# Kernel optimization log

Hardware: AMD Instinct MI355X
Metric: run time of the kernel (lower is better)

The kernel has to match this reference:

```python
import jax, jax.numpy as jnp
import numpy as np

B, S, H = 2, 2048, 1024
NUM_HEAD = 16
HEAD = H // NUM_HEAD
NEG = -10000000000.0


def setup_inputs() -> dict:
    key = jax.random.key(0)
    ks = jax.random.split(key, 10)
    scale = 1.0 / np.sqrt(H)
    return {
        "query": jax.random.normal(ks[0], (B, S, H), jnp.float32),
        "key": jax.random.normal(ks[1], (B, S, H), jnp.float32),
        "value": jax.random.normal(ks[2], (B, S, H), jnp.float32),
        "mask": jax.random.randint(ks[3], (B, S), 0, 2, jnp.int32),
        "Wq": jax.random.normal(ks[4], (H, H), jnp.float32) * scale,
        "bq": jnp.zeros((H,), jnp.float32),
        "Wk": jax.random.normal(ks[5], (H, H), jnp.float32) * scale,
        "bk": jnp.zeros((H,), jnp.float32),
        "Wv": jax.random.normal(ks[6], (H, H), jnp.float32) * scale,
        "bv": jnp.zeros((H,), jnp.float32),
    }


def reference(query, key, value, mask, Wq, bq, Wk, bk, Wv, bv):
    b, s, h = query.shape
    # Linear projections (torch Linear: x @ W.T + b), split into heads -> [b, nh, s, hd]
    def proj(x, W, bias):
        y = x @ W.T + bias
        return y.reshape(b, s, NUM_HEAD, HEAD).transpose(0, 2, 1, 3)

    q = proj(query, Wq, bq)
    k = proj(key, Wk, bk)
    v = proj(value, Wv, bv)

    # NOTE: original module has NO 1/sqrt(head_dim) scaling -- faithful.
    attn_score = jnp.einsum("bhqd,bhkd->bhqk", q, k)  # [b, nh, s, s]
    # key-padding mask bias: 0 where mask==1, -1e10 where mask==0, broadcast over query dim
    bias_add = jnp.where(mask[:, None, None, :] == 0, NEG, 0.0).astype(attn_score.dtype)
    attn_score = attn_score + bias_add
    attn_ratio = jax.nn.softmax(attn_score, axis=-1)
    out = jnp.einsum("bhqk,bhkd->bhqd", attn_ratio, v)  # [b, nh, s, hd]
    out = out.transpose(0, 2, 1, 3).reshape(b, s, h)
    # Dropout is identity in eval mode; output_linear is defined but never used in forward.
    return out
```

## Files before the change

### kernel.cpp

```cpp
#include <hip/hip_runtime.h>

#define BATCH 2
#define S_LEN 2048
#define HDIM  1024
#define NHEAD 16
#define HD    64
#define NEGBIAS -1e10f
#define LOG2E 1.44269504088896f

typedef __attribute__((ext_vector_type(8))) _Float16 half8;
typedef __attribute__((ext_vector_type(4))) _Float16 half4;
typedef __attribute__((ext_vector_type(4))) float   f32x4;
typedef __attribute__((ext_vector_type(2))) __fp16 fp16x2;
typedef __attribute__((ext_vector_type(4))) __fp16 fp16x4;
typedef __attribute__((ext_vector_type(8))) __fp16 fp16x8;

__device__ __forceinline__ float max3f(float a, float b, float c) {
    return fmaxf(fmaxf(a, b), c);
}

__global__ __launch_bounds__(256) void proj_gemm_f16(
    const float* __restrict__ Xq, const float* __restrict__ Wq, const float* __restrict__ bq,
    const float* __restrict__ Xk, const float* __restrict__ Wk, const float* __restrict__ bk,
    const float* __restrict__ Xv, const float* __restrict__ Wv, const float* __restrict__ bv,
    _Float16* __restrict__ Qb, _Float16* __restrict__ Kb, _Float16* __restrict__ Vtb)
{
    const int l  = blockIdx.x;
    const int x  = l & 7;
    const int j  = l >> 3;
    const int mt_ = x * 4 + (j & 3);
    const int nt_ = (j >> 2) & 7;
    const int z   = j >> 5;

    const float* X    = (z == 0) ? Xq : (z == 1) ? Xk : Xv;
    const float* W    = (z == 0) ? Wq : (z == 1) ? Wk : Wv;
    const float* bias = (z == 0) ? bq : (z == 1) ? bk : bv;
    _Float16* Y       = (z == 0) ? Qb : (z == 1) ? Kb : Vtb;

    const int n0 = nt_ * 128;
    const int m0 = mt_ * 128;

    __shared__ __align__(16) _Float16 As[128][40];
    __shared__ __align__(16) _Float16 Bs[128][40];

    const int t    = threadIdx.x;
    const int w    = t >> 6;
    const int lane = t & 63;
    const int quad = lane >> 4;
    const int lc   = lane & 15;
    const int wm   = (w >> 1) * 64;
    const int wn   = (w & 1) * 64;

    const f32x4 fzero = {0.f, 0.f, 0.f, 0.f};
    f32x4 acc[4][4];
#pragma unroll
    for (int i = 0; i < 4; i++)
#pragma unroll
        for (int j2 = 0; j2 < 4; j2++) acc[i][j2] = fzero;

    const int srow = t >> 2;
    const int sc   = t & 3;

    float4 xa0[2][2], wa0[2][2], xa1[2][2], wa1[2][2];

#define PROJ_ISSUE(K0, XA, WA)                                                \
    {                                                                         \
        _Pragma("unroll")                                                     \
        for (int hf = 0; hf < 2; hf++) {                                      \
            const float* gx = X + (size_t)(m0 + srow + hf * 64) * HDIM + (K0) + sc * 8; \
            XA[hf][0] = *(const float4*)gx;                                   \
            XA[hf][1] = *(const float4*)(gx + 4);                             \
            const float* gw = W + (size_t)(n0 + srow + hf * 64) * HDIM + (K0) + sc * 8; \
            WA[hf][0] = *(const float4*)gw;                                   \
            WA[hf][1] = *(const float4*)(gw + 4);                             \
        }                                                                     \
    }

#define PK8(dst, f0, f1)                                                      \
    {                                                                         \
        fp16x2 p0 = __builtin_amdgcn_cvt_pkrtz((f0).x, (f0).y);               \
        fp16x2 p1 = __builtin_amdgcn_cvt_pkrtz((f0).z, (f0).w);               \
        fp16x2 p2 = __builtin_amdgcn_cvt_pkrtz((f1).x, (f1).y);               \
        fp16x2 p3 = __builtin_amdgcn_cvt_pkrtz((f1).z, (f1).w);               \
        fp16x4 lo = __builtin_shufflevector(p0, p1, 0, 1, 2, 3);              \
        fp16x4 hi = __builtin_shufflevector(p2, p3, 0, 1, 2, 3);              \
        fp16x8 v8 = __builtin_shufflevector(lo, hi, 0, 1, 2, 3, 4, 5, 6, 7);  \
        dst = __builtin_bit_cast(half8, v8);                                  \
    }

#define PROJ_STAGE(XA, WA)                                                    \
    {                                                                         \
        _Pragma("unroll")                                                     \
        for (int hf = 0; hf < 2; hf++) {                                      \
            int row = srow + hf * 64;                                         \
            half8 vx, vw;                                                     \
            PK8(vx, XA[hf][0], XA[hf][1])                                     \
            PK8(vw, WA[hf][0], WA[hf][1])                                     \
            *(half8*)&As[row][sc * 8] = vx;                                   \
            *(half8*)&Bs[row][sc * 8] = vw;                                   \
        }                                                                     \
    }

#define PROJ_COMPUTE                                                          \
    {                                                                         \
        half8 af[4], bf[4];                                                   \
        _Pragma("unroll")                                                     \
        for (int mt = 0; mt < 4; mt++)                                        \
            af[mt] = *(const half8*)&As[wm + mt * 16 + lc][quad * 8];         \
        _Pragma("unroll")                                                     \
        for (int nt = 0; nt < 4; nt++)                                        \
            bf[nt] = *(const half8*)&Bs[wn + nt * 16 + lc][quad * 8];         \
        _Pragma("unroll")                                                     \
        for (int mt = 0; mt < 4; mt++)                                        \
            _Pragma("unroll")                                                 \
            for (int nt = 0; nt < 4; nt++)                                    \
                acc[mt][nt] = __builtin_amdgcn_mfma_f32_16x16x32_f16(         \
                    af[mt], bf[nt], acc[mt][nt], 0, 0, 0);                    \
    }

    PROJ_ISSUE(0,  xa0, wa0)
    PROJ_ISSUE(32, xa1, wa1)

    for (int k0 = 0; k0 < HDIM; k0 += 64) {
        if (k0) __syncthreads();
        PROJ_STAGE(xa0, wa0)
        __syncthreads();
        if (k0 + 64 < HDIM) PROJ_ISSUE(k0 + 64, xa0, wa0)
        PROJ_COMPUTE

        __syncthreads();
        PROJ_STAGE(xa1, wa1)
        __syncthreads();
        if (k0 + 96 < HDIM) PROJ_ISSUE(k0 + 96, xa1, wa1)
        PROJ_COMPUTE
    }

#pragma unroll
    for (int nt = 0; nt < 4; nt++) {
        const int n = n0 + wn + nt * 16 + lc;
        const float bv_ = bias[n];
        const int h = n >> 6, d = n & 63;
#pragma unroll
        for (int mt = 0; mt < 4; mt++) {
#pragma unroll
            for (int r = 0; r < 4; r++) {
                const int m = m0 + wm + mt * 16 + quad * 4 + r;
                const int b = m >> 11, s = m & (S_LEN - 1);
                const int bh = b * NHEAD + h;
                float y = acc[mt][nt][r] + bv_;
                if (z == 0) y *= LOG2E;
                _Float16 val = (_Float16)y;
                if (z == 2)
                    Y[((size_t)bh * HD + d) * S_LEN + s] = val;
                else
                    Y[((size_t)bh * S_LEN + s) * HD + d] = val;
            }
        }
    }
}

__global__ __launch_bounds__(256) void flash_attn_mfma(
    const _Float16* __restrict__ Qb, const _Float16* __restrict__ Kb,
    const _Float16* __restrict__ Vtb, const int* __restrict__ mask,
    float* __restrict__ out)
{
    const int bid = blockIdx.x;
    const int swz = (bid & 7) * 64 + (bid >> 3);
    const int qt = swz & 15;
    const int bh = swz >> 4;
    const int b  = bh >> 4;
    const int h  = bh & (NHEAD - 1);

    __shared__ __align__(16) _Float16 Ks [64][72];
    __shared__ __align__(16) _Float16 Vts[64][72];
    __shared__ __align__(16) _Float16 Ps [4][32][72];
    __shared__ float biasS[64];

    const int t    = threadIdx.x;
    const int w    = t >> 6;
    const int lane = t & 63;
    const int quad = lane >> 4;
    const int lc   = lane & 15;

    const _Float16* Kbase = Kb  + (size_t)bh * S_LEN * HD;
    const _Float16* Vbase = Vtb + (size_t)bh * HD * S_LEN;
    const int* mbase = mask + b * S_LEN;

    half8 qf[2][2];
#pragma unroll
    for (int qg = 0; qg < 2; qg++) {
        const int qrow = qt * 128 + w * 32 + qg * 16 + lc;
#pragma unroll
        for (int s = 0; s < 2; s++)
            qf[qg][s] = *(const half8*)(Qb + ((size_t)bh * S_LEN + qrow) * HD
                                        + s * 32 + quad * 8);
    }

    f32x4 o[2][4];
    const f32x4 fzero = {0.f, 0.f, 0.f, 0.f};
#pragma unroll
    for (int qg = 0; qg < 2; qg++)
#pragma unroll
        for (int nt = 0; nt < 4; nt++) o[qg][nt] = fzero;
    float mrun[2] = {-3.0e38f, -3.0e38f};
    float lrun[2] = {0.f, 0.f};

    const int rr0 = t >> 3,          cc0 = (t & 7) * 8;
    const int rr1 = (t + 256) >> 3;

    half8 kpre[2], vpre[2];
    int   mpre;
#define ATTN_ISSUE(KT)                                                        \
    {                                                                         \
        kpre[0] = *(const half8*)(Kbase + (size_t)((KT) + rr0) * HD + cc0);   \
        kpre[1] = *(const half8*)(Kbase + (size_t)((KT) + rr1) * HD + cc0);   \
        vpre[0] = *(const half8*)(Vbase + (size_t)rr0 * S_LEN + (KT) + cc0);  \
        vpre[1] = *(const half8*)(Vbase + (size_t)rr1 * S_LEN + (KT) + cc0);  \
        mpre    = mbase[(KT) + (t & 63)];                                     \
    }

    ATTN_ISSUE(0)

    for (int kt = 0; kt < S_LEN; kt += 64) {
        if (kt) __syncthreads();
        *(half8*)&Ks [rr0][cc0] = kpre[0];
        *(half8*)&Ks [rr1][cc0] = kpre[1];
        *(half8*)&Vts[rr0][cc0] = vpre[0];
        *(half8*)&Vts[rr1][cc0] = vpre[1];
        if (t < 64) biasS[t] = mpre ? 0.f : NEGBIAS;
        __syncthreads();

        if (kt + 64 < S_LEN) ATTN_ISSUE(kt + 64)

        f32x4 scf[2][4];
#pragma unroll
        for (int tt = 0; tt < 4; tt++) {
            float4 b4 = *(const float4*)&biasS[tt * 16 + quad * 4];
            f32x4 cini = {b4.x, b4.y, b4.z, b4.w};
            scf[0][tt] = cini;
            scf[1][tt] = cini;
        }
#pragma unroll
        for (int s = 0; s < 2; s++) {
#pragma unroll
            for (int tt = 0; tt < 4; tt++) {
                half8 kf = *(const half8*)&Ks[tt * 16 + lc][s * 32 + quad * 8];
                scf[0][tt] = __builtin_amdgcn_mfma_f32_16x16x32_f16(kf, qf[0][s], scf[0][tt], 0, 0, 0);
                scf[1][tt] = __builtin_amdgcn_mfma_f32_16x16x32_f16(kf, qf[1][s], scf[1][tt], 0, 0, 0);
            }
        }

#pragma unroll
        for (int qg = 0; qg < 2; qg++) {
            const f32x4 a0 = scf[qg][0], a1 = scf[qg][1],
                        a2 = scf[qg][2], a3 = scf[qg][3];
            float m0 = max3f(a0[0], a0[1], a0[2]);
            float m1 = max3f(a0[3], a1[0], a1[1]);
            float m2 = max3f(a1[2], a1[3], a2[0]);
            float m3 = max3f(a2[1], a2[2], a2[3]);
            float m4 = max3f(a3[0], a3[1], a3[2]);
            float mx = fmaxf(max3f(m0, m1, m2), max3f(m3, m4, a3[3]));
            mx = fmaxf(mx, __shfl_xor(mx, 16));
            mx = fmaxf(mx, __shfl_xor(mx, 32));

            if (!__all(mx <= mrun[qg] + 8.f)) {
                float mn = fmaxf(mrun[qg], mx);
                float al = __builtin_amdgcn_exp2f(mrun[qg] - mn);
                lrun[qg] *= al;
#pragma unroll
                for (int nt = 0; nt < 4; nt++) {
                    o[qg][nt][0] *= al; o[qg][nt][1] *= al;
                    o[qg][nt][2] *= al; o[qg][nt][3] *= al;
                }
                mrun[qg] = mn;
            }

            const float mr = mrun[qg];
            float ps[4][4];
#pragma unroll
            for (int tt = 0; tt < 4; tt++)
#pragma unroll
                for (int r = 0; r < 4; r++) {
                    float p = __builtin_amdgcn_exp2f(scf[qg][tt][r] - mr);
                    ps[tt][r] = p;
                }
            float s0 = (ps[0][0] + ps[0][1]) + (ps[0][2] + ps[0][3]);
            float s1 = (ps[1][0] + ps[1][1]) + (ps[1][2] + ps[1][3]);
            float s2 = (ps[2][0] + ps[2][1]) + (ps[2][2] + ps[2][3]);
            float s3 = (ps[3][0] + ps[3][1]) + (ps[3][2] + ps[3][3]);
            float ls = (s0 + s1) + (s2 + s3);
            ls += __shfl_xor(ls, 16);
            ls += __shfl_xor(ls, 32);
            lrun[qg] += ls;

#pragma unroll
            for (int tt = 0; tt < 4; tt++) {
                fp16x2 p01 = __builtin_amdgcn_cvt_pkrtz(ps[tt][0], ps[tt][1]);
                fp16x2 p23 = __builtin_amdgcn_cvt_pkrtz(ps[tt][2], ps[tt][3]);
                fp16x4 pk4 = __builtin_shufflevector(p01, p23, 0, 1, 2, 3);
                *(half4*)&Ps[w][qg * 16 + lc][tt * 16 + quad * 4] =
                    __builtin_bit_cast(half4, pk4);
            }
        }

#pragma unroll
        for (int s = 0; s < 2; s++) {
            half8 pf0 = *(const half8*)&Ps[w][lc]     [s * 32 + quad * 8];
            half8 pf1 = *(const half8*)&Ps[w][16 + lc][s * 32 + quad * 8];
#pragma unroll
            for (int nt = 0; nt < 4; nt++) {
                half8 vf = *(const half8*)&Vts[nt * 16 + lc][s * 32 + quad * 8];
                o[0][nt] = __builtin_amdgcn_mfma_f32_16x16x32_f16(vf, pf0, o[0][nt], 0, 0, 0);
                o[1][nt] = __builtin_amdgcn_mfma_f32_16x16x32_f16(vf, pf1, o[1][nt], 0, 0, 0);
            }
        }
    }

#pragma unroll
    for (int qg = 0; qg < 2; qg++) {
        const int qrow = qt * 128 + w * 32 + qg * 16 + lc;
        const float inv = 1.f / lrun[qg];
        const size_t rowb = ((size_t)b * S_LEN + qrow) * HDIM + h * HD;
#pragma unroll
        for (int nt = 0; nt < 4; nt++) {
            float4 v;
            v.x = o[qg][nt][0] * inv; v.y = o[qg][nt][1] * inv;
            v.z = o[qg][nt][2] * inv; v.w = o[qg][nt][3] * inv;
            *(float4*)&out[rowb + nt * 16 + quad * 4] = v;
        }
    }
}

extern "C" void kernel_launch(void* const* d_in, const int* in_sizes, int n_in,
                              void* d_out, int out_size, void* d_ws, size_t ws_size,
                              hipStream_t stream) {
    const float* query = (const float*)d_in[0];
    const float* key   = (const float*)d_in[1];
    const float* value = (const float*)d_in[2];
    const int*   mask  = (const int*)  d_in[3];
    const float* Wq    = (const float*)d_in[4];
    const float* bq    = (const float*)d_in[5];
    const float* Wk    = (const float*)d_in[6];
    const float* bk    = (const float*)d_in[7];
    const float* Wv    = (const float*)d_in[8];
    const float* bv    = (const float*)d_in[9];
    float* out = (float*)d_out;

    const size_t nElem = (size_t)BATCH * S_LEN * HDIM;
    if (ws_size < 3 * nElem * sizeof(_Float16)) return;
    _Float16* Qb  = (_Float16*)d_ws;
    _Float16* Kb  = Qb + nElem;
    _Float16* Vtb = Kb + nElem;

    proj_gemm_f16<<<768, 256, 0, stream>>>(query, Wq, bq, key, Wk, bk,
                                           value, Wv, bv, Qb, Kb, Vtb);

    flash_attn_mfma<<<BATCH * NHEAD * (S_LEN / 128), 256, 0, stream>>>(
        Qb, Kb, Vtb, mask, out);
}
```

Measured before the change: 236.3 us.

## Stage projection GEMM tiles via direct global-to-LDS loads with XOR swizzle

The QKV projection GEMM now copies fp32 X and W tiles straight from global memory into LDS with global_load_lds, double-buffered, instead of loading into registers, converting to fp16 and then storing to LDS. The fp16 conversion moves to the LDS read side, and a XOR swizzle on columns is meant to avoid bank conflicts. The goal is to cut register pressure and the number of barriers per k-step, and to let loads overlap with MFMA work. In exchange, LDS use doubles because it holds fp32 and two buffers, and every wave repeats the conversion work on each read.

```diff
diff --git a/kernel.cpp b/kernel.cpp
--- a/kernel.cpp
+++ b/kernel.cpp
@@ -18,6 +18,24 @@
 __device__ __forceinline__ float max3f(float a, float b, float c) {
     return fmaxf(fmaxf(a, b), c);
 }
+
+__device__ __forceinline__ void gload16(const float* g, float* l) {
+    __builtin_amdgcn_global_load_lds(
+        (const __attribute__((address_space(1))) unsigned int*)g,
+        (__attribute__((address_space(3))) unsigned int*)l, 16, 0, 0);
+}
+
+#define PK8V(dst, lo, hi)                                                     \
+    {                                                                         \
+        fp16x2 p0 = __builtin_amdgcn_cvt_pkrtz((lo)[0], (lo)[1]);             \
+        fp16x2 p1 = __builtin_amdgcn_cvt_pkrtz((lo)[2], (lo)[3]);             \
+        fp16x2 p2 = __builtin_amdgcn_cvt_pkrtz((hi)[0], (hi)[1]);             \
+        fp16x2 p3 = __builtin_amdgcn_cvt_pkrtz((hi)[2], (hi)[3]);             \
+        fp16x4 l4 = __builtin_shufflevector(p0, p1, 0, 1, 2, 3);              \
+        fp16x4 h4 = __builtin_shufflevector(p2, p3, 0, 1, 2, 3);              \
+        fp16x8 v8 = __builtin_shufflevector(l4, h4, 0, 1, 2, 3, 4, 5, 6, 7);  \
+        dst = __builtin_bit_cast(half8, v8);                                  \
+    }
 
 __global__ __launch_bounds__(256) void proj_gemm_f16(
     const float* __restrict__ Xq, const float* __restrict__ Wq, const float* __restrict__ bq,
@@ -40,8 +58,8 @@
     const int n0 = nt_ * 128;
     const int m0 = mt_ * 128;
 
-    __shared__ __align__(16) _Float16 As[128][40];
-    __shared__ __align__(16) _Float16 Bs[128][40];
+    __shared__ __align__(16) float As[2][128 * 32];
+    __shared__ __align__(16) float Bs[2][128 * 32];
 
     const int t    = threadIdx.x;
     const int w    = t >> 6;
@@ -58,58 +76,42 @@
 #pragma unroll
         for (int j2 = 0; j2 < 4; j2++) acc[i][j2] = fzero;
 
-    const int srow = t >> 2;
-    const int sc   = t & 3;
-
-    float4 xa0[2][2], wa0[2][2], xa1[2][2], wa1[2][2];
-
-#define PROJ_ISSUE(K0, XA, WA)                                                \
+    const int lr  = lane >> 3;
+    const int lcx = (lane & 7) ^ lr;
+    const float* gA = X + (size_t)(m0 + w * 32 + lr) * HDIM + lcx * 4;
+    const float* gB = W + (size_t)(n0 + w * 32 + lr) * HDIM + lcx * 4;
+    const int ach = w * 1024;
+
+#define PROJ_STAGE(BUF, K0)                                                   \
     {                                                                         \
         _Pragma("unroll")                                                     \
-        for (int hf = 0; hf < 2; hf++) {                                      \
-            const float* gx = X + (size_t)(m0 + srow + hf * 64) * HDIM + (K0) + sc * 8; \
-            XA[hf][0] = *(const float4*)gx;                                   \
-            XA[hf][1] = *(const float4*)(gx + 4);                             \
-            const float* gw = W + (size_t)(n0 + srow + hf * 64) * HDIM + (K0) + sc * 8; \
-            WA[hf][0] = *(const float4*)gw;                                   \
-            WA[hf][1] = *(const float4*)(gw + 4);                             \
+        for (int c = 0; c < 4; c++) {                                         \
+            gload16(gA + (K0) + c * 8192, &As[BUF][ach + c * 256]);           \
+            gload16(gB + (K0) + c * 8192, &Bs[BUF][ach + c * 256]);           \
         }                                                                     \
     }
 
-#define PK8(dst, f0, f1)                                                      \
-    {                                                                         \
-        fp16x2 p0 = __builtin_amdgcn_cvt_pkrtz((f0).x, (f0).y);               \
-        fp16x2 p1 = __builtin_amdgcn_cvt_pkrtz((f0).z, (f0).w);               \
-        fp16x2 p2 = __builtin_amdgcn_cvt_pkrtz((f1).x, (f1).y);               \
-        fp16x2 p3 = __builtin_amdgcn_cvt_pkrtz((f1).z, (f1).w);               \
-        fp16x4 lo = __builtin_shufflevector(p0, p1, 0, 1, 2, 3);              \
-        fp16x4 hi = __builtin_shufflevector(p2, p3, 0, 1, 2, 3);              \
-        fp16x8 v8 = __builtin_shufflevector(lo, hi, 0, 1, 2, 3, 4, 5, 6, 7);  \
-        dst = __builtin_bit_cast(half8, v8);                                  \
-    }
-
-#define PROJ_STAGE(XA, WA)                                                    \
-    {                                                                         \
-        _Pragma("unroll")                                                     \
-        for (int hf = 0; hf < 2; hf++) {                                      \
-            int row = srow + hf * 64;                                         \
-            half8 vx, vw;                                                     \
-            PK8(vx, XA[hf][0], XA[hf][1])                                     \
-            PK8(vw, WA[hf][0], WA[hf][1])                                     \
-            *(half8*)&As[row][sc * 8] = vx;                                   \
-            *(half8*)&Bs[row][sc * 8] = vw;                                   \
-        }                                                                     \
-    }
-
-#define PROJ_COMPUTE                                                          \
+    const int xr   = lc & 7;
+    const int arow = (wm + lc) * 32;
+    const int brow = (wn + lc) * 32;
+    const int ac0  = ((quad * 2)     ^ xr) * 4;
+    const int ac1  = ((quad * 2 + 1) ^ xr) * 4;
+
+#define PROJ_COMPUTE(BUF)                                                     \
     {                                                                         \
         half8 af[4], bf[4];                                                   \
         _Pragma("unroll")                                                     \
-        for (int mt = 0; mt < 4; mt++)                                        \
-            af[mt] = *(const half8*)&As[wm + mt * 16 + lc][quad * 8];         \
+        for (int mt = 0; mt < 4; mt++) {                                      \
+            f32x4 lo = *(const f32x4*)&As[BUF][arow + mt * 512 + ac0];        \
+            f32x4 hi = *(const f32x4*)&As[BUF][arow + mt * 512 + ac1];        \
+            PK8V(af[mt], lo, hi)                                              \
+        }                                                                     \
         _Pragma("unroll")                                                     \
-        for (int nt = 0; nt < 4; nt++)                                        \
-            bf[nt] = *(const half8*)&Bs[wn + nt * 16 + lc][quad * 8];         \
+        for (int nt = 0; nt < 4; nt++) {                                      \
+            f32x4 lo = *(const f32x4*)&Bs[BUF][brow + nt * 512 + ac0];        \
+            f32x4 hi = *(const f32x4*)&Bs[BUF][brow + nt * 512 + ac1];        \
+            PK8V(bf[nt], lo, hi)                                              \
+        }                                                                     \
         _Pragma("unroll")                                                     \
         for (int mt = 0; mt < 4; mt++)                                        \
             _Pragma("unroll")                                                 \
@@ -118,21 +120,16 @@
                     af[mt], bf[nt], acc[mt][nt], 0, 0, 0);                    \
     }
 
-    PROJ_ISSUE(0,  xa0, wa0)
-    PROJ_ISSUE(32, xa1, wa1)
+    PROJ_STAGE(0, 0)
+    __syncthreads();
 
     for (int k0 = 0; k0 < HDIM; k0 += 64) {
-        if (k0) __syncthreads();
-        PROJ_STAGE(xa0, wa0)
+        if (k0 + 32 < HDIM) PROJ_STAGE(1, k0 + 32)
+        PROJ_COMPUTE(0)
         __syncthreads();
-        if (k0 + 64 < HDIM) PROJ_ISSUE(k0 + 64, xa0, wa0)
-        PROJ_COMPUTE
-
+        if (k0 + 64 < HDIM) PROJ_STAGE(0, k0 + 64)
+        PROJ_COMPUTE(1)
         __syncthreads();
-        PROJ_STAGE(xa1, wa1)
-        __syncthreads();
-        if (k0 + 96 < HDIM) PROJ_ISSUE(k0 + 96, xa1, wa1)
-        PROJ_COMPUTE
     }
 
 #pragma unroll
```

After: 253.7 us. 7.4% more time.

## Double-buffer LDS in projection GEMM and use a plain 3D launch grid

Applied to the files above, without the earlier changes.

The projection GEMM now keeps two LDS buffers for the A and B tiles. This cuts the barriers per 64-wide k step from four to two, and the next global loads are issued before each barrier rather than after it. The swizzled 1D block index mapping is replaced by a plain 3D grid (n tile, m tile, which projection), which changes the order in which blocks touch X and W in L2. LDS use per block doubles, which may lower occupancy, and the new block order could hurt cache locality compared with the old swizzle.

```diff
diff --git a/kernel.cpp b/kernel.cpp
--- a/kernel.cpp
+++ b/kernel.cpp
@@ -19,29 +19,34 @@
     return fmaxf(fmaxf(a, b), c);
 }
 
+__device__ __forceinline__ half8 pk8(float4 a, float4 b) {
+    fp16x2 p0 = __builtin_amdgcn_cvt_pkrtz(a.x, a.y);
+    fp16x2 p1 = __builtin_amdgcn_cvt_pkrtz(a.z, a.w);
+    fp16x2 p2 = __builtin_amdgcn_cvt_pkrtz(b.x, b.y);
+    fp16x2 p3 = __builtin_amdgcn_cvt_pkrtz(b.z, b.w);
+    fp16x4 lo = __builtin_shufflevector(p0, p1, 0, 1, 2, 3);
+    fp16x4 hi = __builtin_shufflevector(p2, p3, 0, 1, 2, 3);
+    fp16x8 v8 = __builtin_shufflevector(lo, hi, 0, 1, 2, 3, 4, 5, 6, 7);
+    return __builtin_bit_cast(half8, v8);
+}
+
 __global__ __launch_bounds__(256) void proj_gemm_f16(
     const float* __restrict__ Xq, const float* __restrict__ Wq, const float* __restrict__ bq,
     const float* __restrict__ Xk, const float* __restrict__ Wk, const float* __restrict__ bk,
     const float* __restrict__ Xv, const float* __restrict__ Wv, const float* __restrict__ bv,
     _Float16* __restrict__ Qb, _Float16* __restrict__ Kb, _Float16* __restrict__ Vtb)
 {
-    const int l  = blockIdx.x;
-    const int x  = l & 7;
-    const int j  = l >> 3;
-    const int mt_ = x * 4 + (j & 3);
-    const int nt_ = (j >> 2) & 7;
-    const int z   = j >> 5;
-
+    const int z = blockIdx.z;
     const float* X    = (z == 0) ? Xq : (z == 1) ? Xk : Xv;
     const float* W    = (z == 0) ? Wq : (z == 1) ? Wk : Wv;
     const float* bias = (z == 0) ? bq : (z == 1) ? bk : bv;
     _Float16* Y       = (z == 0) ? Qb : (z == 1) ? Kb : Vtb;
 
-    const int n0 = nt_ * 128;
-    const int m0 = mt_ * 128;
-
-    __shared__ __align__(16) _Float16 As[128][40];
-    __shared__ __align__(16) _Float16 Bs[128][40];
+    const int n0 = blockIdx.x * 128;
+    const int m0 = blockIdx.y * 128;
+
+    __shared__ __align__(16) _Float16 As[2][128][40];
+    __shared__ __align__(16) _Float16 Bs[2][128][40];
 
     const int t    = threadIdx.x;
     const int w    = t >> 6;
@@ -76,40 +81,25 @@
         }                                                                     \
     }
 
-#define PK8(dst, f0, f1)                                                      \
-    {                                                                         \
-        fp16x2 p0 = __builtin_amdgcn_cvt_pkrtz((f0).x, (f0).y);               \
-        fp16x2 p1 = __builtin_amdgcn_cvt_pkrtz((f0).z, (f0).w);               \
-        fp16x2 p2 = __builtin_amdgcn_cvt_pkrtz((f1).x, (f1).y);               \
-        fp16x2 p3 = __builtin_amdgcn_cvt_pkrtz((f1).z, (f1).w);               \
-        fp16x4 lo = __builtin_shufflevector(p0, p1, 0, 1, 2, 3);              \
-        fp16x4 hi = __builtin_shufflevector(p2, p3, 0, 1, 2, 3);              \
-        fp16x8 v8 = __builtin_shufflevector(lo, hi, 0, 1, 2, 3, 4, 5, 6, 7);  \
-        dst = __builtin_bit_cast(half8, v8);                                  \
-    }
-
-#define PROJ_STAGE(XA, WA)                                                    \
+#define PROJ_STAGE(BUF, XA, WA)                                               \
     {                                                                         \
         _Pragma("unroll")                                                     \
         for (int hf = 0; hf < 2; hf++) {                                      \
             int row = srow + hf * 64;                                         \
-            half8 vx, vw;                                                     \
-            PK8(vx, XA[hf][0], XA[hf][1])                                     \
-            PK8(vw, WA[hf][0], WA[hf][1])                                     \
-            *(half8*)&As[row][sc * 8] = vx;                                   \
-            *(half8*)&Bs[row][sc * 8] = vw;                                   \
+            *(half8*)&As[BUF][row][sc * 8] = pk8(XA[hf][0], XA[hf][1]);       \
+            *(half8*)&Bs[BUF][row][sc * 8] = pk8(WA[hf][0], WA[hf][1]);       \
         }                                                                     \
     }
 
-#define PROJ_COMPUTE                                                          \
+#define PROJ_COMP(BUF)                                                        \
     {                                                                         \
         half8 af[4], bf[4];                                                   \
         _Pragma("unroll")                                                     \
         for (int mt = 0; mt < 4; mt++)                                        \
-            af[mt] = *(const half8*)&As[wm + mt * 16 + lc][quad * 8];         \
+            af[mt] = *(const half8*)&As[BUF][wm + mt * 16 + lc][quad * 8];    \
         _Pragma("unroll")                                                     \
         for (int nt = 0; nt < 4; nt++)                                        \
-            bf[nt] = *(const half8*)&Bs[wn + nt * 16 + lc][quad * 8];         \
+            bf[nt] = *(const half8*)&Bs[BUF][wn + nt * 16 + lc][quad * 8];    \
         _Pragma("unroll")                                                     \
         for (int mt = 0; mt < 4; mt++)                                        \
             _Pragma("unroll")                                                 \
@@ -122,17 +112,14 @@
     PROJ_ISSUE(32, xa1, wa1)
 
     for (int k0 = 0; k0 < HDIM; k0 += 64) {
-        if (k0) __syncthreads();
-        PROJ_STAGE(xa0, wa0)
+        PROJ_STAGE(0, xa0, wa0)
+        if (k0 + 64 < HDIM) PROJ_ISSUE(k0 + 64, xa0, wa0)
         __syncthreads();
-        if (k0 + 64 < HDIM) PROJ_ISSUE(k0 + 64, xa0, wa0)
-        PROJ_COMPUTE
-
+        PROJ_COMP(0)
+        PROJ_STAGE(1, xa1, wa1)
+        if (k0 + 96 < HDIM) PROJ_ISSUE(k0 + 96, xa1, wa1)
         __syncthreads();
-        PROJ_STAGE(xa1, wa1)
-        __syncthreads();
-        if (k0 + 96 < HDIM) PROJ_ISSUE(k0 + 96, xa1, wa1)
-        PROJ_COMPUTE
+        PROJ_COMP(1)
     }
 
 #pragma unroll
@@ -352,8 +339,9 @@
     _Float16* Kb  = Qb + nElem;
     _Float16* Vtb = Kb + nElem;
 
-    proj_gemm_f16<<<768, 256, 0, stream>>>(query, Wq, bq, key, Wk, bk,
-                                           value, Wv, bv, Qb, Kb, Vtb);
+    dim3 gproj(HDIM / 128, (BATCH * S_LEN) / 128, 3);
+    proj_gemm_f16<<<gproj, 256, 0, stream>>>(query, Wq, bq, key, Wk, bk,
+                                             value, Wv, bv, Qb, Kb, Vtb);
 
     flash_attn_mfma<<<BATCH * NHEAD * (S_LEN / 128), 256, 0, stream>>>(
         Qb, Kb, Vtb, mask, out);
```

After: 243.9 us. 3.2% more time.
